# Kernel optimization log

Hardware: AMD Instinct MI355X
Metric: run time of the kernel (lower is better)

Reference implementation:

```python
import jax, jax.numpy as jnp
import numpy as np

N, E, G, DIM, XF, EF = 50000, 800000, 512, 64, 28, 3

def setup_inputs():
    key = jax.random.key(0)
    ks = iter(jax.random.split(key, 64))
    def nrm(shape, scale=0.1):
        return jax.random.normal(next(ks), shape, dtype=jnp.float32) * scale
    inp = {}
    inp["x"] = jax.random.normal(next(ks), (N, XF), dtype=jnp.float32)
    inp["edge_attr"] = jax.random.normal(next(ks), (E, EF), dtype=jnp.float32)
    # conv1: bond_encoder 3->28->28, mlp 28->28->DIM
    inp["c1_be1"] = nrm((EF, XF)); inp["c1_be2"] = nrm((XF, XF))
    inp["c1_m1"] = nrm((XF, XF)); inp["c1_m2"] = nrm((XF, DIM))
    inp["c1_eps"] = jnp.zeros((1,), jnp.float32)
    # conv2: bond_encoder 3->DIM->DIM, mlp DIM->DIM->DIM
    inp["c2_be1"] = nrm((EF, DIM)); inp["c2_be2"] = nrm((DIM, DIM))
    inp["c2_m1"] = nrm((DIM, DIM)); inp["c2_m2"] = nrm((DIM, DIM))
    inp["c2_eps"] = jnp.zeros((1,), jnp.float32)
    # conv3 (reused for layer 4, as in the source)
    inp["c3_be1"] = nrm((EF, DIM)); inp["c3_be2"] = nrm((DIM, DIM))
    inp["c3_m1"] = nrm((DIM, DIM)); inp["c3_m2"] = nrm((DIM, DIM))
    inp["c3_eps"] = jnp.zeros((1,), jnp.float32)
    for i in (1, 2, 3, 4):
        inp["bn%d_g" % i] = jnp.ones((DIM,), jnp.float32) + nrm((DIM,), 0.01)
        inp["bn%d_b" % i] = nrm((DIM,), 0.01)
        inp["bn%d_m" % i] = nrm((DIM,), 0.1)
        inp["bn%d_v" % i] = jnp.ones((DIM,), jnp.float32) + jax.random.uniform(next(ks), (DIM,), dtype=jnp.float32)
    inp["fc1_w"] = nrm((4 * DIM, DIM)); inp["fc1_b"] = jnp.zeros((DIM,), jnp.float32)
    inp["fc2_w"] = nrm((DIM, DIM)); inp["fc2_b"] = jnp.zeros((DIM,), jnp.float32)
    inp["fc3_w"] = nrm((DIM, DIM)); inp["fc3_b"] = jnp.zeros((DIM,), jnp.float32)
    inp["fc4_w"] = nrm((DIM, 1)); inp["fc4_b"] = jnp.zeros((1,), jnp.float32)
    inp["edge_index"] = jax.random.randint(next(ks), (2, E), 0, N, dtype=jnp.int32)
    inp["batch"] = jnp.sort(jax.random.randint(next(ks), (N,), 0, G, dtype=jnp.int32))
    return inp

def reference(x, edge_attr, c1_be1, c1_be2, c1_m1, c1_m2, c1_eps, c2_be1, c2_be2, c2_m1, c2_m2, c2_eps, c3_be1, c3_be2, c3_m1, c3_m2, c3_eps, bn1_g, bn1_b, bn1_m, bn1_v, bn2_g, bn2_b, bn2_m, bn2_v, bn3_g, bn3_b, bn3_m, bn3_v, bn4_g, bn4_b, bn4_m, bn4_v, fc1_w, fc1_b, fc2_w, fc2_b, fc3_w, fc3_b, fc4_w, fc4_b, edge_index, batch):
    n = x.shape[0]
    src, dst = edge_index[0], edge_index[1]
    def gin(h, be1, be2, m1, m2, eps):
        e = jnp.maximum(edge_attr @ be1, 0.0) @ be2            # bond encoder [E, d]
        msg = jnp.maximum(h[src] + e, 0.0)                     # edge gather + relu
        agg = jax.ops.segment_sum(msg, dst, num_segments=n)    # scatter-add aggregate
        z = (1.0 + eps) * h + agg
        return jnp.maximum(z @ m1, 0.0) @ m2                   # node MLP
    def bn(h, g, b, m, v):                                     # BatchNorm1d (eval)
        return (h - m) * (g * jax.lax.rsqrt(v + 1e-5)) + b
    x1 = bn(jnp.maximum(gin(x,  c1_be1, c1_be2, c1_m1, c1_m2, c1_eps), 0.0), bn1_g, bn1_b, bn1_m, bn1_v)
    x2 = bn(jnp.maximum(gin(x1, c2_be1, c2_be2, c2_m1, c2_m2, c2_eps), 0.0), bn2_g, bn2_b, bn2_m, bn2_v)
    x3 = bn(jnp.maximum(gin(x2, c3_be1, c3_be2, c3_m1, c3_m2, c3_eps), 0.0), bn3_g, bn3_b, bn3_m, bn3_v)
    x4 = bn(jnp.maximum(gin(x3, c3_be1, c3_be2, c3_m1, c3_m2, c3_eps), 0.0), bn4_g, bn4_b, bn4_m, bn4_v)  # conv3 reused, faithful to source
    cat = jnp.concatenate([x1, x2, x3, x4], axis=-1)           # [N, 4*DIM]
    cnt = jax.ops.segment_sum(jnp.ones((n,), cat.dtype), batch, num_segments=G)
    pooled = jax.ops.segment_sum(cat, batch, num_segments=G) / jnp.maximum(cnt, 1.0)[:, None]
    h = jnp.maximum(pooled @ fc1_w + fc1_b, 0.0)
    h = jnp.maximum(h @ fc2_w + fc2_b, 0.0)
    h = jnp.maximum(h @ fc3_w + fc3_b, 0.0)
    return (h @ fc4_w + fc4_b).reshape(-1)
```

## Files before the change

### kernel.cpp

```cpp
#include <hip/hip_runtime.h>


typedef __attribute__((ext_vector_type(8))) short short8v;
typedef __attribute__((ext_vector_type(4))) float float4v;

__device__ __forceinline__ unsigned short f2bf(float f) {
  unsigned u = __float_as_uint(f);
  u += 0x7fff + ((u >> 16) & 1);
  return (unsigned short)(u >> 16);
}
__device__ __forceinline__ float bf2f(unsigned short s) {
  return __uint_as_float(((unsigned)s) << 16);
}
__device__ __forceinline__ float4v mfma16(short8v a, short8v b, float4v c) {
  return __builtin_amdgcn_mfma_f32_16x16x32_bf16(a, b, c, 0, 0, 0);
}

__global__ __launch_bounds__(256) void prep_kernel(
    const float* c1be2, const float* c2be2, const float* c3be2,
    const float* c1m1, const float* c2m1, const float* c3m1,
    const float* c1m2, const float* c2m2, const float* c3m2,
    const float* c1be1, const float* c2be1, const float* c3be1,
    unsigned short* FB, float* B1P) {
  int job = blockIdx.x;
  if (job < 9) {
    const float* W = nullptr; int ldw = 0, kmax = 0, nmax = 0, NT = 0, KT = 0;
    switch (job) {
      case 0: W = c1be2; ldw = 28; kmax = 28; nmax = 28; NT = 2; KT = 1; break;
      case 1: W = c2be2; ldw = 64; kmax = 64; nmax = 64; NT = 4; KT = 2; break;
      case 2: W = c3be2; ldw = 64; kmax = 64; nmax = 64; NT = 4; KT = 2; break;
      case 3: W = c1m1;  ldw = 28; kmax = 28; nmax = 28; NT = 2; KT = 1; break;
      case 4: W = c2m1;  ldw = 64; kmax = 64; nmax = 64; NT = 4; KT = 2; break;
      case 5: W = c3m1;  ldw = 64; kmax = 64; nmax = 64; NT = 4; KT = 2; break;
      case 6: W = c1m2;  ldw = 64; kmax = 28; nmax = 64; NT = 4; KT = 1; break;
      case 7: W = c2m2;  ldw = 64; kmax = 64; nmax = 64; NT = 4; KT = 2; break;
      case 8: W = c3m2;  ldw = 64; kmax = 64; nmax = 64; NT = 4; KT = 2; break;
    }
    unsigned short* out = FB + (size_t)job * 4096;
    int total = NT * KT * 512;
    for (int i = threadIdx.x; i < total; i += 256) {
      int fi = i >> 9, l = (i >> 3) & 63, j = i & 7;
      int kt = fi % KT, nt = fi / KT;
      int k = kt * 32 + (l >> 4) * 8 + j;
      int n = nt * 16 + (l & 15);
      float w = (k < kmax && n < nmax) ? W[k * ldw + n] : 0.f;
      out[i] = f2bf(w);
    }
  } else {
    int b = job - 9;
    const float* be1 = (b == 0) ? c1be1 : (b == 1) ? c2be1 : c3be1;
    int DE = (b == 0) ? 28 : 64;
    float* out = B1P + (size_t)b * (64 * 48);
    for (int i = threadIdx.x; i < 64 * 48; i += 256) {
      int l = i / 48, r = i % 48;
      int c = r / 16, kk = r % 16;
      int kt = kk >> 3, j = kk & 7;
      int k = kt * 32 + ((l >> 4) & 3) * 8 + j;
      out[i] = (k < DE) ? be1[c * DE + k] : 0.f;
    }
  }
}


__global__ void hist_kernel(const int* __restrict__ idx, int* __restrict__ cnt, int n) {
  int i = blockIdx.x * blockDim.x + threadIdx.x;
  int stride = gridDim.x * blockDim.x;
  for (; i < n; i += stride) atomicAdd(&cnt[idx[i]], 1);
}

__global__ void fill_perm_kernel(const int* __restrict__ srcs, const int* __restrict__ dsts,
                                 const float* __restrict__ eattr, int* __restrict__ cursor,
                                 int* __restrict__ src_s, float4* __restrict__ attr_s,
                                 int n) {
  int i = blockIdx.x * blockDim.x + threadIdx.x;
  int stride = gridDim.x * blockDim.x;
  for (; i < n; i += stride) {
    int d = dsts[i];
    int p = atomicAdd(&cursor[d], 1);
    src_s[p] = srcs[i];
    attr_s[p] = make_float4(eattr[i * 3 + 0], eattr[i * 3 + 1], eattr[i * 3 + 2], 0.f);
  }
}

__global__ __launch_bounds__(256) void block_reduce_kernel(
    const int* __restrict__ cnt, int* __restrict__ bsum, int n) {
  __shared__ int s[256];
  int i = blockIdx.x * 256 + threadIdx.x;
  s[threadIdx.x] = (i < n) ? cnt[i] : 0;
  __syncthreads();
  for (int d = 128; d > 0; d >>= 1) {
    if (threadIdx.x < d) s[threadIdx.x] += s[threadIdx.x + d];
    __syncthreads();
  }
  if (threadIdx.x == 0) bsum[blockIdx.x] = s[0];
}

__global__ __launch_bounds__(256) void bsum_scan_kernel(int* __restrict__ bsum, int nb) {
  __shared__ int s[1024];
  for (int i = threadIdx.x; i < 1024; i += 256) s[i] = (i < nb) ? bsum[i] : 0;
  __syncthreads();
  if (threadIdx.x == 0) {
    int acc = 0;
    for (int i = 0; i < nb; i++) { int t = s[i]; s[i] = acc; acc += t; }
  }
  __syncthreads();
  for (int i = threadIdx.x; i < nb; i += 256) bsum[i] = s[i];
}

__global__ __launch_bounds__(256) void scan_apply_kernel(
    const int* __restrict__ cnt, const int* __restrict__ bsum,
    int* __restrict__ offs, int* __restrict__ cursor, int n) {
  __shared__ int s[256];
  int b = blockIdx.x;
  int i = b * 256 + threadIdx.x;
  int v = (i < n) ? cnt[i] : 0;
  s[threadIdx.x] = v;
  __syncthreads();
  for (int d = 1; d < 256; d <<= 1) {
    int t = (threadIdx.x >= d) ? s[threadIdx.x - d] : 0;
    __syncthreads();
    s[threadIdx.x] += t;
    __syncthreads();
  }
  int excl = s[threadIdx.x] - v + bsum[b];
  if (i < n) { offs[i] = excl; cursor[i] = excl; }
  if (i == n - 1) offs[n] = excl + v;
}

__global__ void boundary_kernel(const int* __restrict__ batch, int* __restrict__ goff,
                                int n, int G) {
  int g = blockIdx.x * blockDim.x + threadIdx.x;
  if (g > G) return;
  int lo = 0, hi = n;
  while (lo < hi) {
    int mid = (lo + hi) >> 1;
    if (batch[mid] < g) lo = mid + 1; else hi = mid;
  }
  goff[g] = lo;
}

template <int DE>
__global__ __launch_bounds__(256) void bond_kernel(
    const float4* __restrict__ attr_s, const float* __restrict__ b1p,
    const unsigned short* __restrict__ be2f, unsigned short* __restrict__ ebond, int E) {
  constexpr int KT = (DE + 31) / 32;
  constexpr int NT = (DE + 15) / 16;
  constexpr int RB = KT * 32;
  int lane = threadIdx.x & 63;
  int nc = lane & 15, rr = (lane >> 4) * 4;
  int gw = (blockIdx.x * blockDim.x + threadIdx.x) >> 6;
  int nw = (gridDim.x * blockDim.x) >> 6;

  float b1v[3][KT * 8];
#pragma unroll
  for (int c = 0; c < 3; c++)
#pragma unroll
    for (int kk = 0; kk < KT * 8; kk++)
      b1v[c][kk] = b1p[lane * 48 + c * 16 + (kk >> 3) * 8 + (kk & 7)];

  short8v bfrag[NT][KT];
#pragma unroll
  for (int nt = 0; nt < NT; nt++)
#pragma unroll
    for (int kt = 0; kt < KT; kt++)
      bfrag[nt][kt] = *(const short8v*)(be2f + ((nt * KT + kt) * 64 + lane) * 8);

  int ntiles = (E + 15) >> 4;
  for (int tile = gw; tile < ntiles; tile += nw) {
    int j0 = tile << 4;
    float4 a = attr_s[min(j0 + nc, E - 1)];
    short8v af[KT];
#pragma unroll
    for (int kt = 0; kt < KT; kt++)
#pragma unroll
      for (int j = 0; j < 8; j++) {
        int kk = kt * 8 + j;
        float t = fmaxf(fmaf(a.x, b1v[0][kk], fmaf(a.y, b1v[1][kk], a.z * b1v[2][kk])), 0.f);
        af[kt][j] = (short)f2bf(t);
      }
    float4v acc[NT];
#pragma unroll
    for (int nt = 0; nt < NT; nt++) {
      acc[nt] = (float4v){0.f, 0.f, 0.f, 0.f};
#pragma unroll
      for (int kt = 0; kt < KT; kt++) acc[nt] = mfma16(af[kt], bfrag[nt][kt], acc[nt]);
    }
#pragma unroll
    for (int nt = 0; nt < NT; nt++)
#pragma unroll
      for (int r = 0; r < 4; r++) {
        int row = j0 + rr + r;
        if (row < E) ebond[(size_t)row * RB + nt * 16 + nc] = f2bf(acc[nt][r]);
      }
  }
}

template <int DH, int RB>
__global__ __launch_bounds__(256) void agg_kernel(
    const float* __restrict__ h, const unsigned short* __restrict__ eb,
    const float* __restrict__ epsp, const int* __restrict__ src_sorted,
    const int* __restrict__ offs, float* __restrict__ zout, int n_nodes, int E) {
  int wid = (blockIdx.x * blockDim.x + threadIdx.x) >> 6;
  int nw = (gridDim.x * blockDim.x) >> 6;
  int lane = threadIdx.x & 63;
  float eps1 = 1.f + epsp[0];
  const bool hl = (DH == 64) || (lane < DH);
  const bool el = (RB == 64) || (lane < RB);

  for (int vb = wid * 4; vb < n_nodes; vb += nw * 4) {
    int o[5];
#pragma unroll
    for (int q = 0; q <= 4; q++) o[q] = offs[min(vb + q, n_nodes)];
    float acc[4];
    int j[4], je[4];
#pragma unroll
    for (int q = 0; q < 4; q++) {
      j[q] = o[q];
      je[q] = o[q + 1];
      bool valid = (vb + q) < n_nodes;
      acc[q] = (valid && hl) ? eps1 * h[(size_t)(vb + q) * DH + lane] : 0.f;
    }
    int steps = max(max(je[0] - j[0], je[1] - j[1]), max(je[2] - j[2], je[3] - j[3]));
    for (int t = 0; t < steps; t++) {
#pragma unroll
      for (int q = 0; q < 4; q++) {
        int jj = j[q] + t;
        bool act = jj < je[q];
        int jc = min(jj, E - 1);
        int s = src_sorted[jc];
        float b = el ? bf2f(eb[(size_t)jc * RB + lane]) : 0.f;
        float hv = hl ? h[(size_t)s * DH + lane] : 0.f;
        float mv = fmaxf(hv + b, 0.f);
        acc[q] += act ? mv : 0.f;
      }
    }
    if (el) {
#pragma unroll
      for (int q = 0; q < 4; q++)
        if ((vb + q) < n_nodes) zout[(size_t)(vb + q) * RB + lane] = acc[q];
    }
  }
}

template <int DIN>
__global__ __launch_bounds__(256) void node_mfma_kernel(
    const float* __restrict__ z, const unsigned short* __restrict__ m1f_g,
    const unsigned short* __restrict__ m2f_g, const float* __restrict__ bng,
    const float* __restrict__ bnb, const float* __restrict__ bnm,
    const float* __restrict__ bnv, float* __restrict__ xout, int n_nodes) {
  constexpr int KT = (DIN + 31) / 32;
  constexpr int NTH = (DIN + 15) / 16;
  constexpr int ZR = KT * 32;
  constexpr int LROW = 64 * 2 + 16;
  __shared__ __attribute__((aligned(16))) char lds_all[4 * 16 * LROW];
  char* yl = lds_all + (threadIdx.x >> 6) * (16 * LROW);
  int lane = threadIdx.x & 63;
  int nc = lane & 15, kg = lane >> 4, rr = kg * 4;
  int gw = (blockIdx.x * blockDim.x + threadIdx.x) >> 6;
  int nw = (gridDim.x * blockDim.x) >> 6;

  short8v m1f[NTH][KT], m2f[4][KT];
#pragma unroll
  for (int nt = 0; nt < NTH; nt++)
#pragma unroll
    for (int kt = 0; kt < KT; kt++)
      m1f[nt][kt] = *(const short8v*)(m1f_g + ((nt * KT + kt) * 64 + lane) * 8);
#pragma unroll
  for (int nt = 0; nt < 4; nt++)
#pragma unroll
    for (int kt = 0; kt < KT; kt++)
      m2f[nt][kt] = *(const short8v*)(m2f_g + ((nt * KT + kt) * 64 + lane) * 8);

  float scv[4], shv[4];
#pragma unroll
  for (int nt = 0; nt < 4; nt++) {
    int f = nt * 16 + nc;
    float sc = bng[f] * rsqrtf(bnv[f] + 1e-5f);
    scv[nt] = sc;
    shv[nt] = bnb[f] - bnm[f] * sc;
  }

  int ntiles = (n_nodes + 15) >> 4;
  for (int tile = gw; tile < ntiles; tile += nw) {
    int v0 = tile << 4;
    int vr = min(v0 + nc, n_nodes - 1);
    short8v af[KT];
#pragma unroll
    for (int kt = 0; kt < KT; kt++) {
      const float* zp = z + (size_t)vr * ZR + kt * 32 + kg * 8;
      float4 z0 = *(const float4*)(zp);
      float4 z1 = *(const float4*)(zp + 4);
      af[kt][0] = (short)f2bf(z0.x); af[kt][1] = (short)f2bf(z0.y);
      af[kt][2] = (short)f2bf(z0.z); af[kt][3] = (short)f2bf(z0.w);
      af[kt][4] = (short)f2bf(z1.x); af[kt][5] = (short)f2bf(z1.y);
      af[kt][6] = (short)f2bf(z1.z); af[kt][7] = (short)f2bf(z1.w);
    }
    float4v acch[NTH];
#pragma unroll
    for (int nt = 0; nt < NTH; nt++) {
      acch[nt] = (float4v){0.f, 0.f, 0.f, 0.f};
#pragma unroll
      for (int kt = 0; kt < KT; kt++) acch[nt] = mfma16(af[kt], m1f[nt][kt], acch[nt]);
    }
#pragma unroll
    for (int nt = 0; nt < NTH; nt++)
#pragma unroll
      for (int r = 0; r < 4; r++)
        *(unsigned short*)(yl + (rr + r) * LROW + (nt * 16 + nc) * 2) =
            f2bf(fmaxf(acch[nt][r], 0.f));
    asm volatile("" ::: "memory");
    short8v af2[KT];
#pragma unroll
    for (int kt = 0; kt < KT; kt++)
      af2[kt] = *(const short8v*)(yl + nc * LROW + kg * 16 + kt * 64);
    float4v acco[4];
#pragma unroll
    for (int nt = 0; nt < 4; nt++) {
      acco[nt] = (float4v){0.f, 0.f, 0.f, 0.f};
#pragma unroll
      for (int kt = 0; kt < KT; kt++) acco[nt] = mfma16(af2[kt], m2f[nt][kt], acco[nt]);
    }
#pragma unroll
    for (int nt = 0; nt < 4; nt++)
#pragma unroll
      for (int r = 0; r < 4; r++) {
        int v = v0 + rr + r;
        if (v < n_nodes)
          xout[(size_t)v * 64 + nt * 16 + nc] =
              fmaf(fmaxf(acco[nt][r], 0.f), scv[nt], shv[nt]);
      }
    asm volatile("" ::: "memory");
  }
}

__global__ __launch_bounds__(256) void pool_kernel(
    const float* __restrict__ x1, const float* __restrict__ x2,
    const float* __restrict__ x3, const float* __restrict__ x4,
    const int* __restrict__ goff, float* __restrict__ pooled, int G) {
  int g = blockIdx.x;
  int c = threadIdx.x;
  int sel = c >> 6, f = c & 63;
  const float* x = (sel == 0) ? x1 : (sel == 1) ? x2 : (sel == 2) ? x3 : x4;
  int s = goff[g], e = goff[g + 1];
  float acc = 0.f;
  for (int v = s; v < e; v++) acc += x[(size_t)v * 64 + f];
  float cnt = (float)(e - s);
  pooled[g * 256 + c] = acc / fmaxf(cnt, 1.0f);
}

__global__ __launch_bounds__(64) void head_kernel(
    const float* __restrict__ pooled,
    const float* __restrict__ w1, const float* __restrict__ b1,
    const float* __restrict__ w2, const float* __restrict__ b2,
    const float* __restrict__ w3, const float* __restrict__ b3,
    const float* __restrict__ w4, const float* __restrict__ b4,
    float* __restrict__ out, int G) {
  int g = blockIdx.x;
  int lane = threadIdx.x;
  __shared__ float sh[256];
  for (int i = lane; i < 256; i += 64) sh[i] = pooled[g * 256 + i];
  __syncthreads();
  float h1 = b1[lane];
#pragma unroll 8
  for (int i = 0; i < 256; i++) h1 = fmaf(sh[i], w1[i * 64 + lane], h1);
  h1 = fmaxf(h1, 0.f);
  __syncthreads();
  sh[lane] = h1;
  __syncthreads();
  float h2 = b2[lane];
#pragma unroll
  for (int i = 0; i < 64; i++) h2 = fmaf(sh[i], w2[i * 64 + lane], h2);
  h2 = fmaxf(h2, 0.f);
  __syncthreads();
  sh[lane] = h2;
  __syncthreads();
  float h3 = b3[lane];
#pragma unroll
  for (int i = 0; i < 64; i++) h3 = fmaf(sh[i], w3[i * 64 + lane], h3);
  h3 = fmaxf(h3, 0.f);
  float p = h3 * w4[lane];
  for (int d = 32; d > 0; d >>= 1) p += __shfl_down(p, d);
  if (lane == 0) out[g] = p + b4[0];
}


extern "C" void kernel_launch(void* const* d_in, const int* in_sizes, int n_in,
                              void* d_out, int out_size, void* d_ws, size_t ws_size,
                              hipStream_t stream) {
  const float* x      = (const float*)d_in[0];
  const float* eattr  = (const float*)d_in[1];
  const float* c1_be1 = (const float*)d_in[2];
  const float* c1_be2 = (const float*)d_in[3];
  const float* c1_m1  = (const float*)d_in[4];
  const float* c1_m2  = (const float*)d_in[5];
  const float* c1_eps = (const float*)d_in[6];
  const float* c2_be1 = (const float*)d_in[7];
  const float* c2_be2 = (const float*)d_in[8];
  const float* c2_m1  = (const float*)d_in[9];
  const float* c2_m2  = (const float*)d_in[10];
  const float* c2_eps = (const float*)d_in[11];
  const float* c3_be1 = (const float*)d_in[12];
  const float* c3_be2 = (const float*)d_in[13];
  const float* c3_m1  = (const float*)d_in[14];
  const float* c3_m2  = (const float*)d_in[15];
  const float* c3_eps = (const float*)d_in[16];
  const float* bn_g[4] = {(const float*)d_in[17], (const float*)d_in[21],
                          (const float*)d_in[25], (const float*)d_in[29]};
  const float* bn_b[4] = {(const float*)d_in[18], (const float*)d_in[22],
                          (const float*)d_in[26], (const float*)d_in[30]};
  const float* bn_m[4] = {(const float*)d_in[19], (const float*)d_in[23],
                          (const float*)d_in[27], (const float*)d_in[31]};
  const float* bn_v[4] = {(const float*)d_in[20], (const float*)d_in[24],
                          (const float*)d_in[28], (const float*)d_in[32]};
  const float* fc1_w = (const float*)d_in[33];
  const float* fc1_b = (const float*)d_in[34];
  const float* fc2_w = (const float*)d_in[35];
  const float* fc2_b = (const float*)d_in[36];
  const float* fc3_w = (const float*)d_in[37];
  const float* fc3_b = (const float*)d_in[38];
  const float* fc4_w = (const float*)d_in[39];
  const float* fc4_b = (const float*)d_in[40];
  const int* eidx  = (const int*)d_in[41];
  const int* batch = (const int*)d_in[42];

  const int N = in_sizes[0] / 28;
  const int E = in_sizes[1] / 3;
  const int G = out_size;
  const int* src = eidx;
  const int* dst = eidx + E;
  float* outf = (float*)d_out;

  char* p = (char*)d_ws;
  auto alloc = [&](size_t bytes) {
    char* r = p;
    p += (bytes + 255) & ~(size_t)255;
    return r;
  };
  const int NBLK = (N + 255) / 256;
  int* counts   = (int*)alloc((size_t)N * 4);
  int* offs     = (int*)alloc((size_t)(N + 1) * 4);
  int* cursor   = (int*)alloc((size_t)N * 4);
  int* bsum     = (int*)alloc((size_t)NBLK * 4);
  int* goff     = (int*)alloc((size_t)(G + 1) * 4);
  int* src_s    = (int*)alloc((size_t)E * 4);
  float4* attr_s = (float4*)alloc((size_t)E * 16);
  unsigned short* FB = (unsigned short*)alloc(9 * 4096 * 2);
  float* B1P    = (float*)alloc(3 * 64 * 48 * 4);
  unsigned short* ebond = (unsigned short*)alloc((size_t)E * 64 * 2);
  float* zbuf   = (float*)alloc((size_t)N * 64 * 4);
  float* x1     = (float*)alloc((size_t)N * 64 * 4);
  float* x2     = (float*)alloc((size_t)N * 64 * 4);
  float* x3     = (float*)alloc((size_t)N * 64 * 4);
  float* x4     = (float*)alloc((size_t)N * 64 * 4);
  float* pooled = (float*)alloc((size_t)G * 256 * 4);
  (void)ws_size; (void)n_in;

  prep_kernel<<<12, 256, 0, stream>>>(c1_be2, c2_be2, c3_be2, c1_m1, c2_m1, c3_m1,
                                      c1_m2, c2_m2, c3_m2, c1_be1, c2_be1, c3_be1,
                                      FB, B1P);
  hipMemsetAsync(counts, 0, (size_t)N * 4, stream);
  hist_kernel<<<1024, 256, 0, stream>>>(dst, counts, E);
  boundary_kernel<<<(G + 128) / 128, 128, 0, stream>>>(batch, goff, N, G);
  block_reduce_kernel<<<NBLK, 256, 0, stream>>>(counts, bsum, N);
  bsum_scan_kernel<<<1, 256, 0, stream>>>(bsum, NBLK);
  scan_apply_kernel<<<NBLK, 256, 0, stream>>>(counts, bsum, offs, cursor, N);
  fill_perm_kernel<<<1024, 256, 0, stream>>>(src, dst, eattr, cursor, src_s, attr_s, E);

  unsigned short* FB_be2[3] = {FB + 0 * 4096, FB + 1 * 4096, FB + 2 * 4096};
  unsigned short* FB_m1[3]  = {FB + 3 * 4096, FB + 4 * 4096, FB + 5 * 4096};
  unsigned short* FB_m2[3]  = {FB + 6 * 4096, FB + 7 * 4096, FB + 8 * 4096};
  float* B1[3] = {B1P, B1P + 64 * 48, B1P + 2 * 64 * 48};

  dim3 blk(256);
  const int AGGB = (N + 15) / 16;
  bond_kernel<28><<<1024, blk, 0, stream>>>(attr_s, B1[0], FB_be2[0], ebond, E);
  agg_kernel<28, 32><<<AGGB, blk, 0, stream>>>(x, ebond, c1_eps, src_s, offs, zbuf, N, E);
  node_mfma_kernel<28><<<512, blk, 0, stream>>>(zbuf, FB_m1[0], FB_m2[0], bn_g[0],
                                                bn_b[0], bn_m[0], bn_v[0], x1, N);
  bond_kernel<64><<<1024, blk, 0, stream>>>(attr_s, B1[1], FB_be2[1], ebond, E);
  agg_kernel<64, 64><<<AGGB, blk, 0, stream>>>(x1, ebond, c2_eps, src_s, offs, zbuf, N, E);
  node_mfma_kernel<64><<<512, blk, 0, stream>>>(zbuf, FB_m1[1], FB_m2[1], bn_g[1],
                                                bn_b[1], bn_m[1], bn_v[1], x2, N);
  bond_kernel<64><<<1024, blk, 0, stream>>>(attr_s, B1[2], FB_be2[2], ebond, E);
  agg_kernel<64, 64><<<AGGB, blk, 0, stream>>>(x2, ebond, c3_eps, src_s, offs, zbuf, N, E);
  node_mfma_kernel<64><<<512, blk, 0, stream>>>(zbuf, FB_m1[2], FB_m2[2], bn_g[2],
                                                bn_b[2], bn_m[2], bn_v[2], x3, N);
  agg_kernel<64, 64><<<AGGB, blk, 0, stream>>>(x3, ebond, c3_eps, src_s, offs, zbuf, N, E);
  node_mfma_kernel<64><<<512, blk, 0, stream>>>(zbuf, FB_m1[2], FB_m2[2], bn_g[3],
                                                bn_b[3], bn_m[3], bn_v[3], x4, N);

  pool_kernel<<<G, blk, 0, stream>>>(x1, x2, x3, x4, goff, pooled, G);
  head_kernel<<<G, 64, 0, stream>>>(pooled, fc1_w, fc1_b, fc2_w, fc2_b, fc3_w,
                                    fc3_b, fc4_w, fc4_b, outf, G);
}
```

Baseline: 710.3 us.

## Fuse source-node gather and ReLU into bond kernel, simplify aggregation

The bond encoder kernel now also gathers h[src] for each edge, adds the bond embedding, applies ReLU and writes the bf16 message per edge. The aggregation kernel becomes a plain contiguous segment sum over the precomputed messages, one wave per node, with no indirect gathers. The intent is to move the random gather into the edge-parallel MFMA kernel, where it can be better parallelised, and to make aggregation purely streaming. The cost is that layer 4 must recompute the bond embeddings instead of reusing them, and messages are rounded to bf16 after the ReLU.

```diff
diff --git a/kernel.cpp b/kernel.cpp
--- a/kernel.cpp
+++ b/kernel.cpp
@@ -140,9 +140,10 @@
 }
 
 template <int DE>
-__global__ __launch_bounds__(256) void bond_kernel(
+__global__ __launch_bounds__(256) void bond_m_kernel(
     const float4* __restrict__ attr_s, const float* __restrict__ b1p,
-    const unsigned short* __restrict__ be2f, unsigned short* __restrict__ ebond, int E) {
+    const unsigned short* __restrict__ be2f, const float* __restrict__ h,
+    const int* __restrict__ src_s, unsigned short* __restrict__ m_out, int E) {
   constexpr int KT = (DE + 31) / 32;
   constexpr int NT = (DE + 15) / 16;
   constexpr int RB = KT * 32;
@@ -165,6 +166,10 @@
     for (int kt = 0; kt < KT; kt++)
       bfrag[nt][kt] = *(const short8v*)(be2f + ((nt * KT + kt) * 64 + lane) * 8);
 
+  bool colv[NT];
+#pragma unroll
+  for (int nt = 0; nt < NT; nt++) colv[nt] = (DE == 64) || (nt * 16 + nc < DE);
+
   int ntiles = (E + 15) >> 4;
   for (int tile = gw; tile < ntiles; tile += nw) {
     int j0 = tile << 4;
@@ -185,59 +190,57 @@
 #pragma unroll
       for (int kt = 0; kt < KT; kt++) acc[nt] = mfma16(af[kt], bfrag[nt][kt], acc[nt]);
     }
-#pragma unroll
-    for (int nt = 0; nt < NT; nt++)
-#pragma unroll
-      for (int r = 0; r < 4; r++) {
-        int row = j0 + rr + r;
-        if (row < E) ebond[(size_t)row * RB + nt * 16 + nc] = f2bf(acc[nt][r]);
+    int s_r[4];
+    bool rv[4];
+#pragma unroll
+    for (int r = 0; r < 4; r++) {
+      int jr = j0 + rr + r;
+      rv[r] = jr < E;
+      s_r[r] = src_s[min(jr, E - 1)];
+    }
+    float hv[4][NT];
+#pragma unroll
+    for (int r = 0; r < 4; r++)
+#pragma unroll
+      for (int nt = 0; nt < NT; nt++)
+        hv[r][nt] = colv[nt] ? h[(size_t)s_r[r] * DE + nt * 16 + nc] : 0.f;
+#pragma unroll
+    for (int r = 0; r < 4; r++) {
+      if (rv[r]) {
+#pragma unroll
+        for (int nt = 0; nt < NT; nt++) {
+          float mv = colv[nt] ? fmaxf(hv[r][nt] + acc[nt][r], 0.f) : 0.f;
+          m_out[(size_t)(j0 + rr + r) * RB + nt * 16 + nc] = f2bf(mv);
+        }
       }
+    }
   }
 }
 
 template <int DH, int RB>
-__global__ __launch_bounds__(256) void agg_kernel(
-    const float* __restrict__ h, const unsigned short* __restrict__ eb,
-    const float* __restrict__ epsp, const int* __restrict__ src_sorted,
-    const int* __restrict__ offs, float* __restrict__ zout, int n_nodes, int E) {
+__global__ __launch_bounds__(256) void aggm_kernel(
+    const float* __restrict__ h, const unsigned short* __restrict__ m,
+    const float* __restrict__ epsp, const int* __restrict__ offs,
+    float* __restrict__ zout, int n_nodes) {
   int wid = (blockIdx.x * blockDim.x + threadIdx.x) >> 6;
   int nw = (gridDim.x * blockDim.x) >> 6;
   int lane = threadIdx.x & 63;
   float eps1 = 1.f + epsp[0];
   const bool hl = (DH == 64) || (lane < DH);
   const bool el = (RB == 64) || (lane < RB);
-
-  for (int vb = wid * 4; vb < n_nodes; vb += nw * 4) {
-    int o[5];
-#pragma unroll
-    for (int q = 0; q <= 4; q++) o[q] = offs[min(vb + q, n_nodes)];
-    float acc[4];
-    int j[4], je[4];
-#pragma unroll
-    for (int q = 0; q < 4; q++) {
-      j[q] = o[q];
-      je[q] = o[q + 1];
-      bool valid = (vb + q) < n_nodes;
-      acc[q] = (valid && hl) ? eps1 * h[(size_t)(vb + q) * DH + lane] : 0.f;
-    }
-    int steps = max(max(je[0] - j[0], je[1] - j[1]), max(je[2] - j[2], je[3] - j[3]));
-    for (int t = 0; t < steps; t++) {
-#pragma unroll
-      for (int q = 0; q < 4; q++) {
-        int jj = j[q] + t;
-        bool act = jj < je[q];
-        int jc = min(jj, E - 1);
-        int s = src_sorted[jc];
-        float b = el ? bf2f(eb[(size_t)jc * RB + lane]) : 0.f;
-        float hv = hl ? h[(size_t)s * DH + lane] : 0.f;
-        float mv = fmaxf(hv + b, 0.f);
-        acc[q] += act ? mv : 0.f;
+  for (int v = wid; v < n_nodes; v += nw) {
+    float acc = hl ? eps1 * h[(size_t)v * DH + lane] : 0.f;
+    int j = offs[v], e1 = offs[v + 1];
+    if (el) {
+      for (; j + 4 <= e1; j += 4) {
+        float b0 = bf2f(m[(size_t)j * RB + lane]);
+        float b1 = bf2f(m[(size_t)(j + 1) * RB + lane]);
+        float b2 = bf2f(m[(size_t)(j + 2) * RB + lane]);
+        float b3 = bf2f(m[(size_t)(j + 3) * RB + lane]);
+        acc += (b0 + b1) + (b2 + b3);
       }
-    }
-    if (el) {
-#pragma unroll
-      for (int q = 0; q < 4; q++)
-        if ((vb + q) < n_nodes) zout[(size_t)(vb + q) * RB + lane] = acc[q];
+      for (; j < e1; j++) acc += bf2f(m[(size_t)j * RB + lane]);
+      zout[(size_t)v * RB + lane] = acc;
     }
   }
 }
@@ -446,7 +449,7 @@
   float4* attr_s = (float4*)alloc((size_t)E * 16);
   unsigned short* FB = (unsigned short*)alloc(9 * 4096 * 2);
   float* B1P    = (float*)alloc(3 * 64 * 48 * 4);
-  unsigned short* ebond = (unsigned short*)alloc((size_t)E * 64 * 2);
+  unsigned short* mbuf = (unsigned short*)alloc((size_t)E * 64 * 2);
   float* zbuf   = (float*)alloc((size_t)N * 64 * 4);
   float* x1     = (float*)alloc((size_t)N * 64 * 4);
   float* x2     = (float*)alloc((size_t)N * 64 * 4);
@@ -472,20 +475,20 @@
   float* B1[3] = {B1P, B1P + 64 * 48, B1P + 2 * 64 * 48};
 
   dim3 blk(256);
-  const int AGGB = (N + 15) / 16;
-  bond_kernel<28><<<1024, blk, 0, stream>>>(attr_s, B1[0], FB_be2[0], ebond, E);
-  agg_kernel<28, 32><<<AGGB, blk, 0, stream>>>(x, ebond, c1_eps, src_s, offs, zbuf, N, E);
+  bond_m_kernel<28><<<2048, blk, 0, stream>>>(attr_s, B1[0], FB_be2[0], x, src_s, mbuf, E);
+  aggm_kernel<28, 32><<<2048, blk, 0, stream>>>(x, mbuf, c1_eps, offs, zbuf, N);
   node_mfma_kernel<28><<<512, blk, 0, stream>>>(zbuf, FB_m1[0], FB_m2[0], bn_g[0],
                                                 bn_b[0], bn_m[0], bn_v[0], x1, N);
-  bond_kernel<64><<<1024, blk, 0, stream>>>(attr_s, B1[1], FB_be2[1], ebond, E);
-  agg_kernel<64, 64><<<AGGB, blk, 0, stream>>>(x1, ebond, c2_eps, src_s, offs, zbuf, N, E);
+  bond_m_kernel<64><<<2048, blk, 0, stream>>>(attr_s, B1[1], FB_be2[1], x1, src_s, mbuf, E);
+  aggm_kernel<64, 64><<<2048, blk, 0, stream>>>(x1, mbuf, c2_eps, offs, zbuf, N);
   node_mfma_kernel<64><<<512, blk, 0, stream>>>(zbuf, FB_m1[1], FB_m2[1], bn_g[1],
                                                 bn_b[1], bn_m[1], bn_v[1], x2, N);
-  bond_kernel<64><<<1024, blk, 0, stream>>>(attr_s, B1[2], FB_be2[2], ebond, E);
-  agg_kernel<64, 64><<<AGGB, blk, 0, stream>>>(x2, ebond, c3_eps, src_s, offs, zbuf, N, E);
+  bond_m_kernel<64><<<2048, blk, 0, stream>>>(attr_s, B1[2], FB_be2[2], x2, src_s, mbuf, E);
+  aggm_kernel<64, 64><<<2048, blk, 0, stream>>>(x2, mbuf, c3_eps, offs, zbuf, N);
   node_mfma_kernel<64><<<512, blk, 0, stream>>>(zbuf, FB_m1[2], FB_m2[2], bn_g[2],
                                                 bn_b[2], bn_m[2], bn_v[2], x3, N);
-  agg_kernel<64, 64><<<AGGB, blk, 0, stream>>>(x3, ebond, c3_eps, src_s, offs, zbuf, N, E);
+  bond_m_kernel<64><<<2048, blk, 0, stream>>>(attr_s, B1[2], FB_be2[2], x3, src_s, mbuf, E);
+  aggm_kernel<64, 64><<<2048, blk, 0, stream>>>(x3, mbuf, c3_eps, offs, zbuf, N);
   node_mfma_kernel<64><<<512, blk, 0, stream>>>(zbuf, FB_m1[2], FB_m2[2], bn_g[3],
                                                 bn_b[3], bn_m[3], bn_v[3], x4, N);
 
```

Measured after the change: 633.6 us. -10.8%, faster.
